# Performance work log

Hardware: AMD Instinct MI355X
Metric: run time of the kernel (lower is better)

The kernel has to match this reference:

```python
import jax, jax.numpy as jnp
import numpy as np

B, N, C = 1, 32768, 256
NH, F, AG, P = 8, 32, 64, 4  # heads, cube side, agent tokens, pool size (P**3==AG)
HD = C // NH


def setup_inputs() -> dict:
    key = jax.random.key(0)
    ks = jax.random.split(key, 4)
    s = 0.02
    return {
        "x": jax.random.normal(ks[0], (B, N, C), jnp.float32),
        "w_qkv": jax.random.normal(ks[1], (3 * C, C), jnp.float32) * s,
        "b_qkv": jnp.zeros((3 * C,), jnp.float32),
        "w_proj": jax.random.normal(ks[2], (C, C), jnp.float32) * s,
        "b_proj": jnp.zeros((C,), jnp.float32),
        "w_dwc": jax.random.normal(ks[3], (C, C, 3, 3, 3), jnp.float32) * s,
        "b_dwc": jnp.zeros((C,), jnp.float32),
    }


def reference(x, w_qkv, b_qkv, w_proj, b_proj, w_dwc, b_dwc):
    scale = HD ** -0.5
    # qkv projection -> (3, B*NH, N, HD), replicating torch reshape/permute exactly
    qkv = x @ w_qkv.T + b_qkv                       # (B, N, 3C)
    qkv = qkv.reshape(B, N, 3, NH, HD)
    qkv = jnp.transpose(qkv, (2, 0, 3, 1, 4)).reshape(3, B * NH, N, HD)
    q, k, v = qkv[0], qkv[1], qkv[2]

    # agent tokens: pool q (note torch's raw reshape interleaves heads into channels)
    q_vol = q.reshape(B, F, F, F, C)                # faithful to torch reshape
    q_vol = jnp.transpose(q_vol, (0, 4, 1, 2, 3))   # (B, C, F, F, F)
    blk = F // P
    A = q_vol.reshape(B, C, P, blk, P, blk, P, blk).mean(axis=(3, 5, 7))  # (B,C,P,P,P)
    A = A.reshape(B, C, AG).transpose(0, 2, 1)      # (B, AG, C)
    A = A.reshape(B, AG, NH, HD).transpose(0, 2, 1, 3).reshape(B * NH, AG, HD)

    # stage 1: agents attend to keys, aggregate values
    agent_attn = jax.nn.softmax((A * scale) @ jnp.swapaxes(k, -2, -1), axis=-1)  # (B*NH, AG, N)
    agent_v = agent_attn @ v                        # (B*NH, AG, HD)
    # stage 2: queries attend to agents
    q_attn = jax.nn.softmax((q * scale) @ jnp.swapaxes(A, -2, -1), axis=-1)      # (B*NH, N, AG)
    o = q_attn @ agent_v                            # (B*NH, N, HD)

    # faithful to torch: transpose(1,2) then raw reshape
    o = jnp.swapaxes(o, 1, 2).reshape(B, N, C)

    # conv residual on v: (B*NH, N, HD) -> (B, C, F, F, F)
    v5 = jnp.swapaxes(v, 1, 2).reshape(B, C, F, F, F)
    conv = jax.lax.conv_general_dilated(
        v5, w_dwc, window_strides=(1, 1, 1), padding="SAME",
        dimension_numbers=("NCDHW", "OIDHW", "NCDHW"))
    conv = conv + b_dwc[None, :, None, None, None]
    o = o + jnp.transpose(conv, (0, 2, 3, 4, 1)).reshape(B, N, C)

    return o @ w_proj.T + b_proj
```

## Files before the change

### kernel.cpp

```cpp
#include <hip/hip_runtime.h>
#include <stdint.h>

typedef unsigned short u16;
typedef __attribute__((ext_vector_type(8))) short bf16x8;
typedef __attribute__((ext_vector_type(4))) float f32x4;

#define KSCALE (0.17677669529663687f / 512.0f)

__device__ __forceinline__ u16 f2b(float f) {
  unsigned u = __float_as_uint(f);
  unsigned r = (u + 0x7fffu + ((u >> 16) & 1u)) >> 16;
  return (u16)r;
}
__device__ __forceinline__ float b2f(u16 s) { return __uint_as_float(((unsigned)s) << 16); }

__device__ __forceinline__ void async16(const void* g, void* l) {
  __builtin_amdgcn_global_load_lds((const __attribute__((address_space(1))) unsigned int*)g,
                                   (__attribute__((address_space(3))) unsigned int*)l, 16, 0, 0);
}

__device__ __forceinline__ bf16x8 frag8(const float* p, float k) {
  float4 f0 = *(const float4*)p, f1 = *(const float4*)(p + 4);
  bf16x8 v;
  v[0] = f2b(f0.x * k); v[1] = f2b(f0.y * k); v[2] = f2b(f0.z * k); v[3] = f2b(f0.w * k);
  v[4] = f2b(f1.x * k); v[5] = f2b(f1.y * k); v[6] = f2b(f1.z * k); v[7] = f2b(f1.w * k);
  return v;
}

__global__ void prep_cast(const float* __restrict__ x, const float* __restrict__ wq,
                          const float* __restrict__ wp, const float* __restrict__ wdwc,
                          u16* __restrict__ Xb, u16* __restrict__ Wqb,
                          u16* __restrict__ Wpb, u16* __restrict__ Wc) {
  int b = blockIdx.x, tid = threadIdx.x;
  if (b < 8448) {
    const float* src; u16* dst; int i;
    if (b < 8192)      { src = x;  dst = Xb;  i = b * 256 + tid; }
    else if (b < 8384) { src = wq; dst = Wqb; i = (b - 8192) * 256 + tid; }
    else               { src = wp; dst = Wpb; i = (b - 8384) * 256 + tid; }
    const float4 v = ((const float4*)src)[i];
    uint2 o;
    o.x = (unsigned)f2b(v.x) | ((unsigned)f2b(v.y) << 16);
    o.y = (unsigned)f2b(v.z) | ((unsigned)f2b(v.w) << 16);
    ((uint2*)dst)[i] = o;
  } else {
    int o = b - 8448;
    __shared__ u16 lds[6912];
    for (int t = tid; t < 6912; t += 256) lds[t] = f2b(wdwc[o * 6912 + t]);
    __syncthreads();
    int ob = ((o >> 4) * 27) * 4096 + (o & 15) * 32;
    for (int idx = tid; idx < 6912; idx += 256) {
      int t = idx >> 8, i = idx & 255;
      Wc[ob + t * 4096 + (i >> 5) * 512 + ((i >> 3) & 3) * 8 + (i & 7)] = lds[i * 27 + t];
    }
  }
}

__global__ void prep_av(const u16* __restrict__ QKV, u16* __restrict__ v5,
                        float* __restrict__ Apre) {
  int b = blockIdx.x, tid = threadIdx.x;
  if (b < 4913) {
    int idx = b * 256 + tid;
    int c8 = idx & 31, vox = idx >> 5;
    int z = vox / 1156, r2 = vox - z * 1156, y = r2 / 34, x = r2 - y * 34;
    bf16x8 val = {0, 0, 0, 0, 0, 0, 0, 0};
    if (z >= 1 && z <= 32 && y >= 1 && y <= 32 && x >= 1 && x <= 32) {
      int n = (z - 1) * 1024 + (y - 1) * 32 + (x - 1);
      val = *(const bf16x8*)(QKV + n * 768 + 512 + c8 * 8);
    }
    *(bf16x8*)(v5 + vox * 256 + c8 * 8) = val;
  } else {
    int b2 = b - 4913;
    int a = b2 >> 3, s = b2 & 7;
    int hp = tid >> 5, dp = tid & 31;
    int p1 = a >> 4, p2 = (a >> 2) & 3, p3 = a & 3;
    float sum = 0.f;
    for (int ui = 0; ui < 64; ++ui) {
      int u = s * 64 + ui;
      int f1 = p1 * 8 + (u >> 6);
      int f2 = p2 * 8 + ((u >> 3) & 7);
      int f3 = p3 * 8 + (u & 7);
      int vox = f1 * 1024 + f2 * 32 + f3;
      int n  = ((vox & 4095) << 3) + hp;
      int cq = ((vox >> 12) << 5) + dp;
      sum += b2f(QKV[n * 768 + cq]);
    }
    atomicAdd(&Apre[(hp * 64 + a) * 32 + dp], sum);
  }
}


__device__ __forceinline__ void stage64(const u16* src, int row0, int ld, int k0,
                                        short* dst, int tid) {
  int wv = tid >> 6, lane = tid & 63;
  int r15 = lane & 15, kc8 = (lane >> 4) * 8;
#pragma unroll
  for (int j = 0; j < 4; ++j) {
    int p = j & 1, g = wv * 2 + (j >> 1);
    async16(src + (row0 + g * 16 + r15) * ld + k0 + p * 32 + kc8, dst + p * 4096 + g * 512);
  }
}

__device__ __forceinline__ void mfma64(const short* As, const short* Bs, int wm, int wn,
                                       int lane, f32x4 acc[4][4]) {
  const int q = lane >> 4, c = lane & 15;
  const int fo = q * 128 + c * 8;
#pragma unroll
  for (int p = 0; p < 2; ++p) {
    bf16x8 a[4], b[4];
#pragma unroll
    for (int mt = 0; mt < 4; ++mt) a[mt] = *(const bf16x8*)&As[p * 4096 + (wm * 4 + mt) * 512 + fo];
#pragma unroll
    for (int nt = 0; nt < 4; ++nt) b[nt] = *(const bf16x8*)&Bs[p * 4096 + (wn * 4 + nt) * 512 + fo];
#pragma unroll
    for (int mt = 0; mt < 4; ++mt)
#pragma unroll
      for (int nt = 0; nt < 4; ++nt)
        acc[mt][nt] = __builtin_amdgcn_mfma_f32_16x16x32_bf16(a[mt], b[nt], acc[mt][nt], 0, 0, 0);
  }
}

__global__ __launch_bounds__(256) void gemm_qkv(const u16* __restrict__ Xb,
                                                const u16* __restrict__ Wq,
                                                const float* __restrict__ bias,
                                                u16* __restrict__ QKV) {
  const int m0 = blockIdx.x * 128, n0 = blockIdx.y * 128;
  const int tid = threadIdx.x, lane = tid & 63, wv = tid >> 6;
  const int wm = wv >> 1, wn = wv & 1, q = lane >> 4, c = lane & 15;
  __shared__ short As[8192], Bs[8192];
  f32x4 acc[4][4] = {};
  for (int kb = 0; kb < 256; kb += 64) {
    stage64(Xb, m0, 256, kb, As, tid);
    stage64(Wq, n0, 256, kb, Bs, tid);
    __syncthreads();
    mfma64(As, Bs, wm, wn, lane, acc);
    __syncthreads();
  }
#pragma unroll
  for (int nt = 0; nt < 4; ++nt) {
    int col = n0 + wn * 64 + nt * 16 + c;
    float bv = bias[col];
#pragma unroll
    for (int mt = 0; mt < 4; ++mt) {
      int row = m0 + wm * 64 + mt * 16 + q * 4;
#pragma unroll
      for (int r = 0; r < 4; ++r) QKV[(row + r) * 768 + col] = f2b(acc[mt][nt][r] + bv);
    }
  }
}

__global__ __launch_bounds__(256) void conv_s1(const u16* __restrict__ v5,
                                               const u16* __restrict__ Wc,
                                               const float* __restrict__ bias,
                                               u16* __restrict__ Xp,
                                               const u16* __restrict__ QKV,
                                               const float* __restrict__ Apre,
                                               float* __restrict__ avac,
                                               float* __restrict__ rsum) {
  extern __shared__ char smem[];
  const int tid = threadIdx.x, lane = tid & 63, wv = tid >> 6;
  const int q = lane >> 4, c = lane & 15;
  if (blockIdx.x < 512) {
    const int bid = blockIdx.x;
    const int xcd = bid & 7, idx = bid >> 3;
    const int n0 = (idx & 1) * 128;
    const int mt_i = xcd * 32 + (idx >> 1);
    const int m0 = mt_i * 128;
    const int z0 = mt_i >> 3, y0 = (mt_i & 7) * 4;
    const int wm = wv >> 1, wn = wv & 1;
    const int r15 = lane & 15, kq8 = (lane >> 4) * 8;
    short* As0 = (short*)smem;
    short* As1 = (short*)smem + 4608;
    f32x4 acc[4][4] = {};
    const u16* Bq = Wc + c * 32 + q * 8;
    const int nb = ((n0 >> 4) + wn * 4) * 27;
    {
      int base = z0 * 1156 + y0 * 34;
      for (int g = wv; g < 9; g += 4) {
        int row = base + g * 16 + r15;
        row = row < 39303 ? row : 39303;
        async16(v5 + row * 256 + kq8, As0 + g * 512);
      }
    }
    __syncthreads();
    short* cur = As0; short* nxt = As1;
    for (int t = 0; t < 72; ++t) {
      const int dzy = t >> 3, panel = t & 7;
      const int tap0 = dzy * 3;
      bf16x8 breg[3][4];
#pragma unroll
      for (int dx = 0; dx < 3; ++dx)
#pragma unroll
        for (int nt = 0; nt < 4; ++nt)
          breg[dx][nt] = *(const bf16x8*)(Bq + ((nb + nt * 27 + tap0 + dx) * 8 + panel) * 512);
      if (t < 71) {
        const int t1 = t + 1, dzy1 = t1 >> 3, panel1 = t1 & 7;
        const int dz1 = dzy1 / 3, dy1 = dzy1 - dz1 * 3;
        const int base1 = (z0 + dz1) * 1156 + (y0 + dy1) * 34;
        const int choff1 = panel1 * 32 + kq8;
        for (int g = wv; g < 9; g += 4) {
          int row = base1 + g * 16 + r15;
          row = row < 39303 ? row : 39303;
          async16(v5 + row * 256 + choff1, nxt + g * 512);
        }
      }
#pragma unroll
      for (int dx = 0; dx < 3; ++dx) {
        bf16x8 a[4];
#pragma unroll
        for (int mt = 0; mt < 4; ++mt) {
          int M = wm * 64 + mt * 16 + c;
          int vx = M + 2 * (M >> 5) + dx;
          a[mt] = *(const bf16x8*)&cur[(vx >> 4) * 512 + q * 128 + (vx & 15) * 8];
        }
#pragma unroll
        for (int mt = 0; mt < 4; ++mt)
#pragma unroll
          for (int nt = 0; nt < 4; ++nt)
            acc[mt][nt] = __builtin_amdgcn_mfma_f32_16x16x32_bf16(a[mt], breg[dx][nt], acc[mt][nt], 0, 0, 0);
      }
      __syncthreads();
      short* tmp = cur; cur = nxt; nxt = tmp;
    }
#pragma unroll
    for (int nt = 0; nt < 4; ++nt) {
      int col = n0 + wn * 64 + nt * 16 + c;
      float bv = bias[col];
#pragma unroll
      for (int mt = 0; mt < 4; ++mt) {
        int row = m0 + wm * 64 + mt * 16 + q * 4;
#pragma unroll
        for (int r = 0; r < 4; ++r) Xp[(row + r) * 256 + col] = f2b(acc[mt][nt][r] + bv);
      }
    }
  } else {
    const int vb = blockIdx.x - 512;
    const int h = vb >> 7, n0 = (vb & 127) * 256;
    u16* E  = (u16*)smem;
    u16* VT = (u16*)(smem + 33792);
    float* RED = (float*)smem;
    {
      const u16* vrow = QKV + (n0 + tid) * 768 + 512 + h * 32;
#pragma unroll
      for (int d8 = 0; d8 < 4; ++d8) {
        bf16x8 v = *(const bf16x8*)(vrow + d8 * 8);
#pragma unroll
        for (int e = 0; e < 8; ++e) VT[(d8 * 8 + e) * 264 + tid] = (u16)v[e];
      }
    }
    const int wv_ = tid >> 6;
    {
      bf16x8 af[4], bf[4];
#pragma unroll
      for (int mt = 0; mt < 4; ++mt)
        af[mt] = frag8(Apre + h * 2048 + (mt * 16 + c) * 32 + q * 8, KSCALE);
#pragma unroll
      for (int nt = 0; nt < 4; ++nt)
        bf[nt] = *(const bf16x8*)(QKV + (n0 + wv_ * 64 + nt * 16 + c) * 768 + 256 + h * 32 + q * 8);
#pragma unroll
      for (int mt = 0; mt < 4; ++mt)
#pragma unroll
        for (int nt = 0; nt < 4; ++nt) {
          f32x4 s = {0.f, 0.f, 0.f, 0.f};
          s = __builtin_amdgcn_mfma_f32_16x16x32_bf16(af[mt], bf[nt], s, 0, 0, 0);
#pragma unroll
          for (int r = 0; r < 4; ++r) {
            int a = mt * 16 + q * 4 + r, nl = wv_ * 64 + nt * 16 + c;
            E[a * 264 + nl] = f2b(__expf(s[r]));
          }
        }
    }
    __syncthreads();
    {
      int a = tid >> 2, seg = tid & 3;
      float sum = 0.f;
      for (int i = 0; i < 64; ++i) sum += b2f(E[a * 264 + seg * 64 + i]);
      sum += __shfl_xor(sum, 1);
      sum += __shfl_xor(sum, 2);
      if (seg == 0) atomicAdd(&rsum[h * 64 + a], sum);
    }
    f32x4 pv[4][2] = {};
#pragma unroll
    for (int ks = 0; ks < 2; ++ks) {
      bf16x8 ap[4], bp[2];
#pragma unroll
      for (int mt = 0; mt < 4; ++mt)
        ap[mt] = *(const bf16x8*)&E[(mt * 16 + c) * 264 + wv_ * 64 + ks * 32 + q * 8];
#pragma unroll
      for (int nt = 0; nt < 2; ++nt)
        bp[nt] = *(const bf16x8*)&VT[(nt * 16 + c) * 264 + wv_ * 64 + ks * 32 + q * 8];
#pragma unroll
      for (int mt = 0; mt < 4; ++mt)
#pragma unroll
        for (int nt = 0; nt < 2; ++nt)
          pv[mt][nt] = __builtin_amdgcn_mfma_f32_16x16x32_bf16(ap[mt], bp[nt], pv[mt][nt], 0, 0, 0);
    }
    __syncthreads();
#pragma unroll
    for (int mt = 0; mt < 4; ++mt)
#pragma unroll
      for (int nt = 0; nt < 2; ++nt)
#pragma unroll
        for (int r = 0; r < 4; ++r)
          RED[wv_ * 2048 + (mt * 16 + q * 4 + r) * 32 + nt * 16 + c] = pv[mt][nt][r];
    __syncthreads();
    for (int idx = tid; idx < 2048; idx += 256) {
      float t = RED[idx] + RED[2048 + idx] + RED[4096 + idx] + RED[6144 + idx];
      atomicAdd(&avac[h * 2048 + idx], t);
    }
  }
}

__global__ __launch_bounds__(256) void gemm_proj(const u16* __restrict__ Xp,
                                                 const u16* __restrict__ Wp,
                                                 const float* __restrict__ bias,
                                                 float* __restrict__ out) {
  const int m0 = blockIdx.x * 128, n0 = blockIdx.y * 128;
  const int tid = threadIdx.x, lane = tid & 63, wv = tid >> 6;
  const int wm = wv >> 1, wn = wv & 1, q = lane >> 4, c = lane & 15;
  __shared__ short As[8192], Bs[8192];
  f32x4 acc[4][4] = {};
  for (int kb = 0; kb < 256; kb += 64) {
    stage64(Xp, m0, 256, kb, As, tid);
    stage64(Wp, n0, 256, kb, Bs, tid);
    __syncthreads();
    mfma64(As, Bs, wm, wn, lane, acc);
    __syncthreads();
  }
#pragma unroll
  for (int nt = 0; nt < 4; ++nt) {
    int col = n0 + wn * 64 + nt * 16 + c;
    float bv = bias[col];
#pragma unroll
    for (int mt = 0; mt < 4; ++mt) {
      int row = m0 + wm * 64 + mt * 16 + q * 4;
#pragma unroll
      for (int r = 0; r < 4; ++r) out[(row + r) * 256 + col] = acc[mt][nt][r] + bv;
    }
  }
}

__global__ __launch_bounds__(256) void s2_attn(const u16* __restrict__ QKV,
                                               const float* __restrict__ Apre,
                                               const float* __restrict__ avac,
                                               const float* __restrict__ rsum,
                                               u16* __restrict__ Xp) {
  const int h = blockIdx.y, n0 = blockIdx.x * 256;
  const int tid = threadIdx.x, lane = tid & 63, wv = tid >> 6;
  const int q = lane >> 4, c = lane & 15;
  extern __shared__ char smem[];
  u16* P = (u16*)smem;
  float* O = (float*)smem;
  u16* AVT = (u16*)(smem + 36864);

  for (int j = 0; j < 8; ++j) {
    int i = j * 256 + tid;
    int a = i >> 5, d = i & 31;
    AVT[d * 72 + a] = f2b(avac[h * 2048 + i] / rsum[h * 64 + a]);
  }

  f32x4 s[4][4];
  {
    bf16x8 af[4], bf[4];
#pragma unroll
    for (int mt = 0; mt < 4; ++mt)
      af[mt] = *(const bf16x8*)(QKV + (n0 + wv * 64 + mt * 16 + c) * 768 + h * 32 + q * 8);
#pragma unroll
    for (int nt = 0; nt < 4; ++nt)
      bf[nt] = frag8(Apre + h * 2048 + (nt * 16 + c) * 32 + q * 8, KSCALE);
#pragma unroll
    for (int mt = 0; mt < 4; ++mt)
#pragma unroll
      for (int nt = 0; nt < 4; ++nt) {
        f32x4 z = {0.f, 0.f, 0.f, 0.f};
        s[mt][nt] = __builtin_amdgcn_mfma_f32_16x16x32_bf16(af[mt], bf[nt], z, 0, 0, 0);
      }
  }
#pragma unroll
  for (int mt = 0; mt < 4; ++mt)
#pragma unroll
    for (int r = 0; r < 4; ++r) {
      float v0 = s[mt][0][r], v1 = s[mt][1][r], v2 = s[mt][2][r], v3 = s[mt][3][r];
      float mx = fmaxf(fmaxf(v0, v1), fmaxf(v2, v3));
      mx = fmaxf(mx, __shfl_xor(mx, 1));
      mx = fmaxf(mx, __shfl_xor(mx, 2));
      mx = fmaxf(mx, __shfl_xor(mx, 4));
      mx = fmaxf(mx, __shfl_xor(mx, 8));
      float e0 = __expf(v0 - mx), e1 = __expf(v1 - mx), e2 = __expf(v2 - mx), e3 = __expf(v3 - mx);
      float sm = e0 + e1 + e2 + e3;
      sm += __shfl_xor(sm, 1);
      sm += __shfl_xor(sm, 2);
      sm += __shfl_xor(sm, 4);
      sm += __shfl_xor(sm, 8);
      float inv = 1.0f / sm;
      int tok = wv * 64 + mt * 16 + q * 4 + r;
      P[tok * 72 +      c] = f2b(e0 * inv);
      P[tok * 72 + 16 + c] = f2b(e1 * inv);
      P[tok * 72 + 32 + c] = f2b(e2 * inv);
      P[tok * 72 + 48 + c] = f2b(e3 * inv);
    }
  __syncthreads();
  f32x4 o[4][2] = {};
#pragma unroll
  for (int ks = 0; ks < 2; ++ks) {
    bf16x8 ap[4], bv[2];
#pragma unroll
    for (int mt = 0; mt < 4; ++mt)
      ap[mt] = *(const bf16x8*)&P[(wv * 64 + mt * 16 + c) * 72 + ks * 32 + q * 8];
#pragma unroll
    for (int nt = 0; nt < 2; ++nt)
      bv[nt] = *(const bf16x8*)&AVT[(nt * 16 + c) * 72 + ks * 32 + q * 8];
#pragma unroll
    for (int mt = 0; mt < 4; ++mt)
#pragma unroll
      for (int nt = 0; nt < 2; ++nt)
        o[mt][nt] = __builtin_amdgcn_mfma_f32_16x16x32_bf16(ap[mt], bv[nt], o[mt][nt], 0, 0, 0);
  }
  __syncthreads();
#pragma unroll
  for (int mt = 0; mt < 4; ++mt)
#pragma unroll
    for (int nt = 0; nt < 2; ++nt)
#pragma unroll
      for (int r = 0; r < 4; ++r)
        O[(nt * 16 + c) * 258 + wv * 64 + mt * 16 + q * 4 + r] = o[mt][nt][r];
  __syncthreads();
  for (int d = 0; d < 32; ++d) {
    int addr = (h * 32 + d) * 32768 + n0 + tid;
    Xp[addr] = f2b(b2f(Xp[addr]) + O[d * 258 + tid]);
  }
}


extern "C" void kernel_launch(void* const* d_in, const int* in_sizes, int n_in,
                              void* d_out, int out_size, void* d_ws, size_t ws_size,
                              hipStream_t stream) {
  const float* x      = (const float*)d_in[0];
  const float* w_qkv  = (const float*)d_in[1];
  const float* b_qkv  = (const float*)d_in[2];
  const float* w_proj = (const float*)d_in[3];
  const float* b_proj = (const float*)d_in[4];
  const float* w_dwc  = (const float*)d_in[5];
  const float* b_dwc  = (const float*)d_in[6];
  float* out = (float*)d_out;
  char* ws = (char*)d_ws;

  u16* Xb   = (u16*)(ws);
  u16* QKV  = (u16*)(ws + 16777216);
  u16* V5   = (u16*)(ws + 67108864);
  u16* Wc   = (u16*)(ws + 87232512);
  u16* Wqb  = (u16*)(ws + 90771456);
  u16* Wpb  = (u16*)(ws + 91164672);
  float* AVAC = (float*)(ws + 91361280);
  float* RSUM = (float*)(ws + 91426816);
  float* APRE = (float*)(ws + 91428864);
  u16* Xp = Xb;

  hipMemsetAsync(AVAC, 0, 65536 + 2048 + 65536, stream);
  prep_cast<<<8704, 256, 0, stream>>>(x, w_qkv, w_proj, w_dwc, Xb, Wqb, Wpb, Wc);
  gemm_qkv<<<dim3(256, 6), 256, 0, stream>>>(Xb, Wqb, b_qkv, QKV);
  prep_av<<<5425, 256, 0, stream>>>(QKV, V5, APRE);
  conv_s1<<<2560, 256, 50688, stream>>>(V5, Wc, b_dwc, Xp, QKV, APRE, AVAC, RSUM);
  s2_attn<<<dim3(128, 8), 256, 41472, stream>>>(QKV, APRE, AVAC, RSUM, Xp);
  gemm_proj<<<dim3(256, 2), 256, 0, stream>>>(Xp, Wpb, b_proj, out);
}
```

Measured before the change: 350.0 us.

## Stage extra halo rows so conv loop covers all dy taps per LDS tile

```diff
diff --git a/kernel.cpp b/kernel.cpp
--- a/kernel.cpp
+++ b/kernel.cpp
@@ -47,10 +47,12 @@
     __shared__ u16 lds[6912];
     for (int t = tid; t < 6912; t += 256) lds[t] = f2b(wdwc[o * 6912 + t]);
     __syncthreads();
-    int ob = ((o >> 4) * 27) * 4096 + (o & 15) * 32;
+    int o16 = o >> 4, co = o & 15;
     for (int idx = tid; idx < 6912; idx += 256) {
       int t = idx >> 8, i = idx & 255;
-      Wc[ob + t * 4096 + (i >> 5) * 512 + ((i >> 3) & 3) * 8 + (i & 7)] = lds[i * 27 + t];
+      int dz = t / 9, rem = t - dz * 9;
+      int panel = i >> 5, q = (i >> 3) & 3, e = i & 7;
+      Wc[(((panel * 3 + dz) * 16 + o16) * 9 + rem) * 512 + co * 32 + q * 8 + e] = lds[i * 27 + t];
     }
   }
 }
@@ -148,14 +150,14 @@
   }
 }
 
-__global__ __launch_bounds__(256) void conv_s1(const u16* __restrict__ v5,
-                                               const u16* __restrict__ Wc,
-                                               const float* __restrict__ bias,
-                                               u16* __restrict__ Xp,
-                                               const u16* __restrict__ QKV,
-                                               const float* __restrict__ Apre,
-                                               float* __restrict__ avac,
-                                               float* __restrict__ rsum) {
+__global__ __launch_bounds__(256, 3) void conv_s1(const u16* __restrict__ v5,
+                                                  const u16* __restrict__ Wc,
+                                                  const float* __restrict__ bias,
+                                                  u16* __restrict__ Xp,
+                                                  const u16* __restrict__ QKV,
+                                                  const float* __restrict__ Apre,
+                                                  float* __restrict__ avac,
+                                                  float* __restrict__ rsum) {
   extern __shared__ char smem[];
   const int tid = threadIdx.x, lane = tid & 63, wv = tid >> 6;
   const int q = lane >> 4, c = lane & 15;
@@ -169,13 +171,13 @@
     const int wm = wv >> 1, wn = wv & 1;
     const int r15 = lane & 15, kq8 = (lane >> 4) * 8;
     short* As0 = (short*)smem;
-    short* As1 = (short*)smem + 4608;
+    short* As1 = (short*)smem + 6656;
     f32x4 acc[4][4] = {};
-    const u16* Bq = Wc + c * 32 + q * 8;
-    const int nb = ((n0 >> 4) + wn * 4) * 27;
+    const u16* BqB = Wc + c * 32 + q * 8;
+    const int o16b = (n0 >> 4) + wn * 4;
     {
-      int base = z0 * 1156 + y0 * 34;
-      for (int g = wv; g < 9; g += 4) {
+      const int base = z0 * 1156 + y0 * 34;
+      for (int g = wv; g < 13; g += 4) {
         int row = base + g * 16 + r15;
         row = row < 39303 ? row : 39303;
         async16(v5 + row * 256 + kq8, As0 + g * 512);
@@ -183,21 +185,18 @@
     }
     __syncthreads();
     short* cur = As0; short* nxt = As1;
-    for (int t = 0; t < 72; ++t) {
-      const int dzy = t >> 3, panel = t & 7;
-      const int tap0 = dzy * 3;
-      bf16x8 breg[3][4];
-#pragma unroll
-      for (int dx = 0; dx < 3; ++dx)
-#pragma unroll
-        for (int nt = 0; nt < 4; ++nt)
-          breg[dx][nt] = *(const bf16x8*)(Bq + ((nb + nt * 27 + tap0 + dx) * 8 + panel) * 512);
-      if (t < 71) {
-        const int t1 = t + 1, dzy1 = t1 >> 3, panel1 = t1 & 7;
-        const int dz1 = dzy1 / 3, dy1 = dzy1 - dz1 * 3;
-        const int base1 = (z0 + dz1) * 1156 + (y0 + dy1) * 34;
-        const int choff1 = panel1 * 32 + kq8;
-        for (int g = wv; g < 9; g += 4) {
+    for (int t = 0; t < 24; ++t) {
+      const int dz = t >> 3, panel = t & 7;
+      const u16* pb = BqB + ((panel * 3 + dz) * 16 + o16b) * 4608;
+      bf16x8 b0[12];
+#pragma unroll
+      for (int j = 0; j < 12; ++j)
+        b0[j] = *(const bf16x8*)(pb + ((j & 3) * 9 + (j >> 2)) * 512);
+      if (t < 23) {
+        const int t1 = t + 1, dz1 = t1 >> 3, p1 = t1 & 7;
+        const int base1 = (z0 + dz1) * 1156 + y0 * 34;
+        const int choff1 = p1 * 32 + kq8;
+        for (int g = wv; g < 13; g += 4) {
           int row = base1 + g * 16 + r15;
           row = row < 39303 ? row : 39303;
           async16(v5 + row * 256 + choff1, nxt + g * 512);
@@ -216,7 +215,49 @@
         for (int mt = 0; mt < 4; ++mt)
 #pragma unroll
           for (int nt = 0; nt < 4; ++nt)
-            acc[mt][nt] = __builtin_amdgcn_mfma_f32_16x16x32_bf16(a[mt], breg[dx][nt], acc[mt][nt], 0, 0, 0);
+            acc[mt][nt] = __builtin_amdgcn_mfma_f32_16x16x32_bf16(a[mt], b0[dx * 4 + nt], acc[mt][nt], 0, 0, 0);
+      }
+      {
+        bf16x8 b1[12];
+#pragma unroll
+        for (int j = 0; j < 12; ++j)
+          b1[j] = *(const bf16x8*)(pb + ((j & 3) * 9 + 3 + (j >> 2)) * 512);
+#pragma unroll
+        for (int dx = 0; dx < 3; ++dx) {
+          bf16x8 a[4];
+#pragma unroll
+          for (int mt = 0; mt < 4; ++mt) {
+            int M = wm * 64 + mt * 16 + c;
+            int vx = 34 + M + 2 * (M >> 5) + dx;
+            a[mt] = *(const bf16x8*)&cur[(vx >> 4) * 512 + q * 128 + (vx & 15) * 8];
+          }
+#pragma unroll
+          for (int mt = 0; mt < 4; ++mt)
+#pragma unroll
+            for (int nt = 0; nt < 4; ++nt)
+              acc[mt][nt] = __builtin_amdgcn_mfma_f32_16x16x32_bf16(a[mt], b1[dx * 4 + nt], acc[mt][nt], 0, 0, 0);
+        }
+      }
+      {
+        bf16x8 b2[12];
+#pragma unroll
+        for (int j = 0; j < 12; ++j)
+          b2[j] = *(const bf16x8*)(pb + ((j & 3) * 9 + 6 + (j >> 2)) * 512);
+#pragma unroll
+        for (int dx = 0; dx < 3; ++dx) {
+          bf16x8 a[4];
+#pragma unroll
+          for (int mt = 0; mt < 4; ++mt) {
+            int M = wm * 64 + mt * 16 + c;
+            int vx = 68 + M + 2 * (M >> 5) + dx;
+            a[mt] = *(const bf16x8*)&cur[(vx >> 4) * 512 + q * 128 + (vx & 15) * 8];
+          }
+#pragma unroll
+          for (int mt = 0; mt < 4; ++mt)
+#pragma unroll
+            for (int nt = 0; nt < 4; ++nt)
+              acc[mt][nt] = __builtin_amdgcn_mfma_f32_16x16x32_bf16(a[mt], b2[dx * 4 + nt], acc[mt][nt], 0, 0, 0);
+        }
       }
       __syncthreads();
       short* tmp = cur; cur = nxt; nxt = tmp;
```

Result: slower. 496.5 us (+41.9%).
